# Kernel optimization log

Measured on AMD Instinct MI355X. Metric: run time of the kernel, lower is better.

Reference implementation:

```python
import jax, jax.numpy as jnp
import numpy as np

USER = 100000
ITEM = 50000
N = USER + ITEM
LATDIM = 64
IMG_DIM = 1024
E_ADJ = 3_000_000
E_IMG = 1_000_000
GNN_LAYERS = 2
RIS_LAMBDA = 1.0
EPS = 1e-12


def spmm(rows, cols, vals, x):
    # sparse [N,N] @ dense [N,D] via gather + segment-sum
    return jax.ops.segment_sum(vals[:, None] * x[cols], rows, num_segments=N)


def setup_inputs() -> dict:
    key = jax.random.key(0)
    ks = jax.random.split(key, 10)
    return {
        "adj_rows": jax.random.randint(ks[0], (E_ADJ,), 0, N, dtype=jnp.int32),
        "adj_cols": jax.random.randint(ks[1], (E_ADJ,), 0, N, dtype=jnp.int32),
        "adj_vals": jax.random.uniform(ks[2], (E_ADJ,), dtype=jnp.float32),
        "img_rows": jax.random.randint(ks[3], (E_IMG,), 0, N, dtype=jnp.int32),
        "img_cols": jax.random.randint(ks[4], (E_IMG,), 0, N, dtype=jnp.int32),
        "img_vals": jax.random.uniform(ks[5], (E_IMG,), dtype=jnp.float32),
        "image_embedding": jax.random.normal(ks[6], (ITEM, IMG_DIM), dtype=jnp.float32),
        "uEmbeds": jax.random.normal(ks[7], (USER, LATDIM), dtype=jnp.float32) * 0.01,
        "iEmbeds": jax.random.normal(ks[8], (ITEM, LATDIM), dtype=jnp.float32) * 0.01,
        "W_trans": jax.random.normal(ks[9], (IMG_DIM, LATDIM), dtype=jnp.float32) * (1.0 / np.sqrt(IMG_DIM)),
        "b_trans": jnp.zeros((LATDIM,), dtype=jnp.float32),
    }


def reference(adj_rows, adj_cols, adj_vals, img_rows, img_cols, img_vals,
              image_embedding, uEmbeds, iEmbeds, W_trans, b_trans):
    # trans == 1: Linear projection of image features
    image_feats = image_embedding @ W_trans + b_trans  # [ITEM, LATDIM]

    # image_adj @ concat(u, i)
    embeds_img_adj = spmm(img_rows, img_cols, img_vals, jnp.concatenate([uEmbeds, iEmbeds], axis=0))

    # F.normalize(image_feats) along dim=1 (L2, eps=1e-12)
    nrm = jnp.linalg.norm(image_feats, axis=1, keepdims=True)
    feats_n = image_feats / jnp.maximum(nrm, EPS)

    embeds_image = spmm(adj_rows, adj_cols, adj_vals, jnp.concatenate([uEmbeds, feats_n], axis=0))
    embeds_image_ = spmm(adj_rows, adj_cols, adj_vals,
                         jnp.concatenate([embeds_image[:USER], iEmbeds], axis=0))
    embeds_image = embeds_image + embeds_image_ + RIS_LAMBDA * embeds_img_adj

    # stacked GCN layers with sum over all layer outputs (including input)
    acc = embeds_image
    cur = embeds_image
    for _ in range(GNN_LAYERS):
        cur = spmm(adj_rows, adj_cols, adj_vals, cur)
        acc = acc + cur

    return acc[:USER], acc[USER:]
```

## Files before the change

kernel.cpp:

```cpp
#include <hip/hip_runtime.h>
#include <hip/hip_fp16.h>

#define USER_N 100000
#define ITEM_N 50000
#define NN (USER_N + ITEM_N)
#define D 64
#define IMGD 1024
#define LDP 68
#define KSPLIT 4
#define KQ (IMGD / KSPLIT)

#define BUCKET_BITS 10
#define BROWS (1 << BUCKET_BITS)
#define NBUCK ((NN + BROWS - 1) >> BUCKET_BITS)
#define CHUNK 4096

typedef _Float16 v4h __attribute__((ext_vector_type(4)));
typedef _Float16 v8h __attribute__((ext_vector_type(8)));
typedef float v4f __attribute__((ext_vector_type(4)));

typedef __attribute__((address_space(1))) unsigned int GU32;
typedef __attribute__((address_space(3))) unsigned int LU32;

__global__ __launch_bounds__(256) void prep_fused(
    const float* __restrict__ uE, const float* __restrict__ iE,
    __half* __restrict__ x0, __half* __restrict__ xBI,
    const float* __restrict__ W, _Float16* __restrict__ Wt16, int cvt_blocks)
{
    if (blockIdx.x < cvt_blocks) {
        const int i = blockIdx.x * 256 + threadIdx.x;
        const int n4u = USER_N * D / 4;
        const int n4 = NN * D / 4;
        if (i >= n4) return;
        const float4 v = (i < n4u) ? reinterpret_cast<const float4*>(uE)[i]
                                   : reinterpret_cast<const float4*>(iE)[i - n4u];
        union { uint2 u2; __half2 h[2]; } o;
        o.h[0] = __floats2half2_rn(v.x, v.y);
        o.h[1] = __floats2half2_rn(v.z, v.w);
        *reinterpret_cast<uint2*>(x0 + (size_t)i * 4) = o.u2;
        if (i >= n4u)
            *reinterpret_cast<uint2*>(xBI + (size_t)(i - n4u) * 4) = o.u2;
    } else {
        const int id = (blockIdx.x - cvt_blocks) * 256 + threadIdx.x;
        if (id >= D * IMGD) return;
        const int c = id >> 10;
        const int k = id & 1023;
        Wt16[id] = (_Float16)W[(size_t)k * D + c];
    }
}

__global__ __launch_bounds__(256) void gemm_g(
    const float* __restrict__ A, const _Float16* __restrict__ Wt16,
    float* __restrict__ P0, float* __restrict__ P123,
    const int* __restrict__ rp, const int2* __restrict__ ev,
    const __half* __restrict__ src, float* __restrict__ out32,
    int gemm_blocks, int g_blocks)
{
    __shared__ float As[32 * KQ];
    const int q = blockIdx.x / 7, r7 = blockIdx.x % 7;
    if (r7 < 4) {
        const int gb = q * 4 + r7;
        if (gb >= gemm_blocks) return;
        const int t = threadIdx.x;
        const int w = t >> 6;
        const int lane = t & 63;
        const int l16 = lane & 15;
        const int g = lane >> 4;
        const int tile = gb >> 2;
        const int ks = gb & 3;
        const int row0 = tile * 32;
        const int kbase = ks * KQ;

#pragma unroll
        for (int i = 0; i < 8; i++) {
            const int r = w * 8 + i;
            const int grow = row0 + r;
            const int garow = grow < ITEM_N ? grow : ITEM_N - 1;
            const int xm = (r & 7) << 4;
            const char* srcp = reinterpret_cast<const char*>(
                A + (size_t)garow * IMGD + kbase) + ((lane * 16) ^ xm);
            __builtin_amdgcn_global_load_lds(
                (GU32*)srcp, (LU32*)&As[r * KQ], 16, 0, 0);
        }
        asm volatile("s_waitcnt vmcnt(0)" ::: "memory");
        __syncthreads();

        const int wr = (w >> 1) * 16;
        const int wc = (w & 1) * 32;
        const int rr = wr + l16;
        const char* rbase = reinterpret_cast<const char*>(&As[rr * KQ]);
        const int xm = (rr & 7) << 4;

        v4f acc[2] = {};
        const _Float16* wb = Wt16 + (size_t)l16 * IMGD + kbase + g * 4;

        for (int c = 0; c < KQ; c += 64) {
            const int cb = c * 4;
            const float4 f0 = *reinterpret_cast<const float4*>(rbase + ((cb + g * 16) ^ xm));
            const float4 f1 = *reinterpret_cast<const float4*>(rbase + ((cb + 64 + g * 16) ^ xm));
            const float4 f2 = *reinterpret_cast<const float4*>(rbase + ((cb + 128 + g * 16) ^ xm));
            const float4 f3 = *reinterpret_cast<const float4*>(rbase + ((cb + 192 + g * 16) ^ xm));
            union { v8h v; v4h h[2]; } af0, af1;
            {
                v4h h;
                h[0] = (_Float16)f0.x; h[1] = (_Float16)f0.y;
                h[2] = (_Float16)f0.z; h[3] = (_Float16)f0.w;
                af0.h[0] = h;
                h[0] = (_Float16)f1.x; h[1] = (_Float16)f1.y;
                h[2] = (_Float16)f1.z; h[3] = (_Float16)f1.w;
                af0.h[1] = h;
                h[0] = (_Float16)f2.x; h[1] = (_Float16)f2.y;
                h[2] = (_Float16)f2.z; h[3] = (_Float16)f2.w;
                af1.h[0] = h;
                h[0] = (_Float16)f3.x; h[1] = (_Float16)f3.y;
                h[2] = (_Float16)f3.z; h[3] = (_Float16)f3.w;
                af1.h[1] = h;
            }
#pragma unroll
            for (int n = 0; n < 2; n++) {
                const _Float16* wp = wb + (size_t)(wc + n * 16) * IMGD + c;
                union { v8h v; v4h h[2]; } bf;
                bf.h[0] = *reinterpret_cast<const v4h*>(wp);
                bf.h[1] = *reinterpret_cast<const v4h*>(wp + 16);
                acc[n] = __builtin_amdgcn_mfma_f32_16x16x32_f16(af0.v, bf.v, acc[n], 0, 0, 0);
                bf.h[0] = *reinterpret_cast<const v4h*>(wp + 32);
                bf.h[1] = *reinterpret_cast<const v4h*>(wp + 48);
                acc[n] = __builtin_amdgcn_mfma_f32_16x16x32_f16(af1.v, bf.v, acc[n], 0, 0, 0);
            }
        }
        float* Cp = (ks == 0) ? P0 : P123 + (size_t)(ks - 1) * ITEM_N * D;
#pragma unroll
        for (int n = 0; n < 2; n++) {
            const int col = wc + n * 16 + l16;
#pragma unroll
            for (int r = 0; r < 4; r++) {
                const int grow = row0 + wr + g * 4 + r;
                if (grow < ITEM_N)
                    Cp[(size_t)grow * D + col] = acc[n][r];
            }
        }
    } else {
        const int sb = q * 3 + (r7 - 4);
        if (sb >= g_blocks) return;
        const int wid = (sb * 256 + threadIdx.x) >> 6;
        const int lane = threadIdx.x & 63;
        const int sub = lane >> 3;
        const int l8 = lane & 7;
        const int rowbase = wid * 8;
        if (rowbase >= NN) return;
        const int row = rowbase + sub;

        int v = 0;
        if (lane <= 8 && rowbase + lane <= NN) v = rp[rowbase + lane];
        const int s = __shfl(v, sub, 64);
        const int e = __shfl(v, sub + 1, 64);

        const __half* srcl = src + l8 * 8;
        float acc[8] = {};

        union cvt4 { uint4 u; __half2 h[4]; };
        int i = s;
        for (; i + 3 < e; i += 4) {
            const int2 E0 = ev[i], E1 = ev[i + 1], E2 = ev[i + 2], E3 = ev[i + 3];
            cvt4 g0, g1, g2, g3;
            g0.u = *reinterpret_cast<const uint4*>(srcl + (size_t)E0.x * D);
            g1.u = *reinterpret_cast<const uint4*>(srcl + (size_t)E1.x * D);
            g2.u = *reinterpret_cast<const uint4*>(srcl + (size_t)E2.x * D);
            g3.u = *reinterpret_cast<const uint4*>(srcl + (size_t)E3.x * D);
#pragma unroll
            for (int k = 0; k < 4; k++) {
                const cvt4& g = k == 0 ? g0 : k == 1 ? g1 : k == 2 ? g2 : g3;
                const float w = __int_as_float(k == 0 ? E0.y : k == 1 ? E1.y
                                               : k == 2 ? E2.y : E3.y);
#pragma unroll
                for (int j = 0; j < 4; j++) {
                    const float2 f = __half22float2(g.h[j]);
                    acc[2 * j]     += w * f.x;
                    acc[2 * j + 1] += w * f.y;
                }
            }
        }
        for (; i < e; i++) {
            const int2 E0 = ev[i];
            cvt4 g;
            g.u = *reinterpret_cast<const uint4*>(srcl + (size_t)E0.x * D);
            const float w = __int_as_float(E0.y);
#pragma unroll
            for (int j = 0; j < 4; j++) {
                const float2 f = __half22float2(g.h[j]);
                acc[2 * j]     += w * f.x;
                acc[2 * j + 1] += w * f.y;
            }
        }

        if (row >= NN) return;
        const size_t idx = (size_t)row * D + l8 * 8;
#pragma unroll
        for (int h = 0; h < 2; h++) {
            float4 o;
            o.x = acc[4 * h]; o.y = acc[4 * h + 1];
            o.z = acc[4 * h + 2]; o.w = acc[4 * h + 3];
            *reinterpret_cast<float4*>(&out32[idx + h * 4]) = o;
        }
    }
}

__global__ __launch_bounds__(256) void gemm_feats32(
    const float* __restrict__ A, const float* __restrict__ W,
    const float* __restrict__ b, float* __restrict__ C)
{
    __shared__ float As[32][LDP];
    __shared__ float Ws[64][LDP];
    const int row0 = blockIdx.x * 32;
    const int t = threadIdx.x;
    const int tx = t & 15, ty = t >> 4;
    float acc[2][4] = {};

    const int lr = t >> 4;
    const int lk = (t & 15) * 4;

    for (int k0 = 0; k0 < IMGD; k0 += 64) {
#pragma unroll
        for (int i = 0; i < 2; i++) {
            const int r = lr + i * 16;
            const int grow = row0 + r;
            float4 v = make_float4(0.f, 0.f, 0.f, 0.f);
            if (grow < ITEM_N)
                v = *reinterpret_cast<const float4*>(&A[(size_t)grow * IMGD + k0 + lk]);
            *reinterpret_cast<float4*>(&As[r][lk]) = v;
        }
#pragma unroll
        for (int i = 0; i < 4; i++) {
            const int kr = lr + i * 16;
            float4 v = *reinterpret_cast<const float4*>(&W[(size_t)(k0 + kr) * D + lk]);
            *reinterpret_cast<float4*>(&Ws[kr][lk]) = v;
        }
        __syncthreads();
#pragma unroll
        for (int kb = 0; kb < 16; kb++) {
            float a_[2][4], w_[4][4];
#pragma unroll
            for (int i = 0; i < 2; i++) {
                const float4 v = *reinterpret_cast<const float4*>(&As[ty * 2 + i][kb * 4]);
                a_[i][0] = v.x; a_[i][1] = v.y; a_[i][2] = v.z; a_[i][3] = v.w;
            }
#pragma unroll
            for (int j = 0; j < 4; j++) {
                const float4 v = *reinterpret_cast<const float4*>(&Ws[kb * 4 + j][tx * 4]);
                w_[j][0] = v.x; w_[j][1] = v.y; w_[j][2] = v.z; w_[j][3] = v.w;
            }
#pragma unroll
            for (int j = 0; j < 4; j++)
#pragma unroll
                for (int i = 0; i < 2; i++)
#pragma unroll
                    for (int c = 0; c < 4; c++)
                        acc[i][c] += a_[i][j] * w_[j][c];
        }
        __syncthreads();
    }
    const float4 bias = *reinterpret_cast<const float4*>(&b[tx * 4]);
#pragma unroll
    for (int i = 0; i < 2; i++) {
        const int grow = row0 + ty * 2 + i;
        if (grow < ITEM_N) {
            float4 v;
            v.x = acc[i][0] + bias.x;
            v.y = acc[i][1] + bias.y;
            v.z = acc[i][2] + bias.z;
            v.w = acc[i][3] + bias.w;
            *reinterpret_cast<float4*>(&C[(size_t)grow * D + tx * 4]) = v;
        }
    }
}

__global__ __launch_bounds__(256) void rownorm_h4(
    const float* __restrict__ P0, const float* __restrict__ P123,
    const float* __restrict__ b, __half* __restrict__ Y, int nrows)
{
    const int gid = blockIdx.x * blockDim.x + threadIdx.x;
    const int row = gid >> 6;
    const int lane = threadIdx.x & 63;
    if (row >= nrows) return;
    const size_t idx = (size_t)row * D + lane;
    const size_t N1 = (size_t)ITEM_N * D;
    float v = P0[idx] + P123[idx] + P123[idx + N1] + P123[idx + 2 * N1] + b[lane];
    float s = v * v;
#pragma unroll
    for (int o = 32; o > 0; o >>= 1) s += __shfl_xor(s, o, 64);
    const float scale = 1.0f / fmaxf(sqrtf(s), 1e-12f);
    Y[idx] = __float2half(v * scale);
}

__global__ __launch_bounds__(256) void rownorm(float* __restrict__ X, int nrows)
{
    const int gid = blockIdx.x * blockDim.x + threadIdx.x;
    const int row = gid >> 6;
    const int lane = threadIdx.x & 63;
    if (row >= nrows) return;
    float v = X[(size_t)row * D + lane];
    float s = v * v;
#pragma unroll
    for (int o = 32; o > 0; o >>= 1) s += __shfl_xor(s, o, 64);
    const float scale = 1.0f / fmaxf(sqrtf(s), 1e-12f);
    X[(size_t)row * D + lane] = v * scale;
}

__global__ __launch_bounds__(256) void bucket_count2(
    const int* __restrict__ rows_a, int nnz_a, int nb_a, int* __restrict__ histT_a,
    const int* __restrict__ rows_b, int nnz_b, int nb_b, int* __restrict__ histT_b)
{
    const bool isA = (int)blockIdx.x < nb_a;
    const int bid = isA ? blockIdx.x : blockIdx.x - nb_a;
    const int* rows = isA ? rows_a : rows_b;
    const int nnz = isA ? nnz_a : nnz_b;
    const int nb = isA ? nb_a : nb_b;
    int* histT = isA ? histT_a : histT_b;

    __shared__ int cnt[NBUCK];
    for (int i = threadIdx.x; i < NBUCK; i += 256) cnt[i] = 0;
    __syncthreads();
    const int e0 = bid * CHUNK;
    const int e1 = min(e0 + CHUNK, nnz);
    for (int e = e0 + threadIdx.x; e < e1; e += 256)
        atomicAdd(&cnt[rows[e] >> BUCKET_BITS], 1);
    __syncthreads();
    for (int b = threadIdx.x; b < NBUCK; b += 256)
        histT[b * nb + bid] = cnt[b];
}

__global__ __launch_bounds__(1024) void scanA2(
    int* __restrict__ histTA, int* __restrict__ bsumsA, int nA, int nsbA,
    int* __restrict__ histTB, int* __restrict__ bsumsB, int nB)
{
    const bool isA = (int)blockIdx.x < nsbA;
    int* cnt = isA ? histTA : histTB;
    int* bsums = isA ? bsumsA : bsumsB;
    const int n = isA ? nA : nB;
    const int bid = isA ? blockIdx.x : blockIdx.x - nsbA;

    const int t = threadIdx.x;
    const int gid = bid * 1024 + t;
    const int lane = t & 63, wid = t >> 6;
    int v = (gid < n) ? cnt[gid] : 0;
    int x = v;
#pragma unroll
    for (int o = 1; o < 64; o <<= 1) {
        int y = __shfl_up(x, o, 64);
        if (lane >= o) x += y;
    }
    __shared__ int ws[16];
    __shared__ int wo[16];
    if (lane == 63) ws[wid] = x;
    __syncthreads();
    if (t < 16) {
        int s = ws[t];
        int xx = s;
#pragma unroll
        for (int o = 1; o < 16; o <<= 1) {
            int y = __shfl_up(xx, o, 16);
            if (t >= o) xx += y;
        }
        wo[t] = xx - s;
        if (t == 15) bsums[bid] = xx;
    }
    __syncthreads();
    if (gid < n) cnt[gid] = x - v + wo[wid];
}

__global__ __launch_bounds__(1024) void scanB2(
    int* __restrict__ bsA, int nbA, int* __restrict__ bsB, int nbB)
{
    int* bs = blockIdx.x == 0 ? bsA : bsB;
    const int nb = blockIdx.x == 0 ? nbA : nbB;
    const int t = threadIdx.x;
    const int lane = t & 63, wid = t >> 6;
    int v = (t < nb) ? bs[t] : 0;
    int x = v;
#pragma unroll
    for (int o = 1; o < 64; o <<= 1) {
        int y = __shfl_up(x, o, 64);
        if (lane >= o) x += y;
    }
    __shared__ int ws[16];
    __shared__ int wo[16];
    if (lane == 63) ws[wid] = x;
    __syncthreads();
    if (t < 16) {
        int s = ws[t];
        int xx = s;
#pragma unroll
        for (int o = 1; o < 16; o <<= 1) {
            int y = __shfl_up(xx, o, 16);
            if (t >= o) xx += y;
        }
        wo[t] = xx - s;
    }
    __syncthreads();
    if (t < nb) bs[t] = x - v + wo[wid];
}

__global__ __launch_bounds__(256) void scan_apply2(
    int* __restrict__ histTA, const int* __restrict__ bsA, int nA,
    int* __restrict__ histTB, const int* __restrict__ bsB, int nB)
{
    const int gid = blockIdx.x * blockDim.x + threadIdx.x;
    if (gid < nA) histTA[gid] += bsA[gid >> 10];
    else if (gid - nA < nB) histTB[gid - nA] += bsB[(gid - nA) >> 10];
}

__global__ __launch_bounds__(256) void bucket_place2(
    const int* __restrict__ rows_a, const int* __restrict__ cols_a,
    const float* __restrict__ vals_a, int nnz_a, int nb_a,
    const int* __restrict__ offsT_a, uint2* __restrict__ rec_a,
    const int* __restrict__ rows_b, const int* __restrict__ cols_b,
    const float* __restrict__ vals_b, int nnz_b, int nb_b,
    const int* __restrict__ offsT_b, uint2* __restrict__ rec_b)
{
    const bool isA = (int)blockIdx.x < nb_a;
    const int bid = isA ? blockIdx.x : blockIdx.x - nb_a;
    const int* rows = isA ? rows_a : rows_b;
    const int* cols = isA ? cols_a : cols_b;
    const float* vals = isA ? vals_a : vals_b;
    const int nnz = isA ? nnz_a : nnz_b;
    const int nb = isA ? nb_a : nb_b;
    const int* offsT = isA ? offsT_a : offsT_b;
    uint2* rec = isA ? rec_a : rec_b;

    __shared__ int cur[NBUCK];
    for (int b = threadIdx.x; b < NBUCK; b += 256)
        cur[b] = offsT[b * nb + bid];
    __syncthreads();
    const int e0 = bid * CHUNK;
    const int e1 = min(e0 + CHUNK, nnz);
    for (int e = e0 + threadIdx.x; e < e1; e += 256) {
        const int r = rows[e];
        const int b = r >> BUCKET_BITS;
        const int pos = atomicAdd(&cur[b], 1);
        rec[pos] = make_uint2(((unsigned)cols[e] << BUCKET_BITS) |
                                  (unsigned)(r & (BROWS - 1)),
                              __float_as_uint(vals[e]));
    }
}

__global__ __launch_bounds__(1024) void bucket_finalize2(
    const uint2* __restrict__ rec_a, int nnz_a, int nb_a,
    const int* __restrict__ offsT_a, int* __restrict__ rp_a, int2* __restrict__ ev_a,
    const uint2* __restrict__ rec_b, int nnz_b, int nb_b,
    const int* __restrict__ offsT_b, int* __restrict__ rp_b, int2* __restrict__ ev_b)
{
    const bool isA = (int)blockIdx.x < NBUCK;
    const int b = isA ? blockIdx.x : blockIdx.x - NBUCK;
    const uint2* rec = isA ? rec_a : rec_b;
    const int nnz = isA ? nnz_a : nnz_b;
    const int nb = isA ? nb_a : nb_b;
    const int* offsT = isA ? offsT_a : offsT_b;
    int* rp = isA ? rp_a : rp_b;
    int2* ev = isA ? ev_a : ev_b;

    const int t = threadIdx.x;
    const int rlo = b << BUCKET_BITS;
    const int segs = offsT[b * nb];
    const int sege = (b + 1 < NBUCK) ? offsT[(b + 1) * nb] : nnz;

    __shared__ int cnt[BROWS];
    __shared__ int cur[BROWS];
    cnt[t] = 0;
    __syncthreads();
    for (int i = segs + t; i < sege; i += 1024)
        atomicAdd(&cnt[rec[i].x & (BROWS - 1)], 1);
    __syncthreads();

    const int lane = t & 63, wid = t >> 6;
    const int v = cnt[t];
    int x = v;
#pragma unroll
    for (int o = 1; o < 64; o <<= 1) {
        int y = __shfl_up(x, o, 64);
        if (lane >= o) x += y;
    }
    __shared__ int wsum[16];
    __shared__ int woff[16];
    if (lane == 63) wsum[wid] = x;
    __syncthreads();
    if (t < 16) {
        int s = wsum[t];
        int xx = s;
#pragma unroll
        for (int o = 1; o < 16; o <<= 1) {
            int y = __shfl_up(xx, o, 16);
            if (t >= o) xx += y;
        }
        woff[t] = xx - s;
    }
    __syncthreads();
    const int start = segs + (x - v + woff[wid]);

    if (rlo + t < NN) rp[rlo + t] = start;
    if (b == NBUCK - 1 && t == 0) rp[NN] = nnz;
    cur[t] = start;
    __syncthreads();

    for (int i = segs + t; i < sege; i += 1024) {
        const uint2 R = rec[i];
        const int rl = (int)(R.x & (BROWS - 1));
        const int c = (int)(R.x >> BUCKET_BITS);
        const int pos = atomicAdd(&cur[rl], 1);
        ev[pos] = make_int2(c, (int)R.y);
    }
}

__global__ __launch_bounds__(256) void spmm_h8(
    const int* __restrict__ rp, const int2* __restrict__ ev,
    const __half* __restrict__ src,
    float* __restrict__ out32, __half* __restrict__ out16, int limit16,
    const float* __restrict__ add1, const float* __restrict__ add2)
{
    const int wid = (blockIdx.x * 256 + threadIdx.x) >> 6;
    const int lane = threadIdx.x & 63;
    const int sub = lane >> 3;
    const int l8 = lane & 7;
    const int rowbase = wid * 8;
    if (rowbase >= NN) return;
    const int row = rowbase + sub;

    int v = 0;
    if (lane <= 8 && rowbase + lane <= NN) v = rp[rowbase + lane];
    const int s = __shfl(v, sub, 64);
    const int e = __shfl(v, sub + 1, 64);

    const __half* srcl = src + l8 * 8;
    float acc[8] = {};

    union cvt4 { uint4 u; __half2 h[4]; };
    int i = s;
    for (; i + 3 < e; i += 4) {
        const int2 E0 = ev[i], E1 = ev[i + 1], E2 = ev[i + 2], E3 = ev[i + 3];
        cvt4 g0, g1, g2, g3;
        g0.u = *reinterpret_cast<const uint4*>(srcl + (size_t)E0.x * D);
        g1.u = *reinterpret_cast<const uint4*>(srcl + (size_t)E1.x * D);
        g2.u = *reinterpret_cast<const uint4*>(srcl + (size_t)E2.x * D);
        g3.u = *reinterpret_cast<const uint4*>(srcl + (size_t)E3.x * D);
#pragma unroll
        for (int k = 0; k < 4; k++) {
            const cvt4& g = k == 0 ? g0 : k == 1 ? g1 : k == 2 ? g2 : g3;
            const float w = __int_as_float(k == 0 ? E0.y : k == 1 ? E1.y
                                           : k == 2 ? E2.y : E3.y);
#pragma unroll
            for (int j = 0; j < 4; j++) {
                const float2 f = __half22float2(g.h[j]);
                acc[2 * j]     += w * f.x;
                acc[2 * j + 1] += w * f.y;
            }
        }
    }
    for (; i < e; i++) {
        const int2 E0 = ev[i];
        cvt4 g;
        g.u = *reinterpret_cast<const uint4*>(srcl + (size_t)E0.x * D);
        const float w = __int_as_float(E0.y);
#pragma unroll
        for (int j = 0; j < 4; j++) {
            const float2 f = __half22float2(g.h[j]);
            acc[2 * j]     += w * f.x;
            acc[2 * j + 1] += w * f.y;
        }
    }

    if (row >= NN) return;
    const size_t idx = (size_t)row * D + l8 * 8;
#pragma unroll
    for (int h = 0; h < 2; h++) {
        if (add1) {
            const float4 a = *reinterpret_cast<const float4*>(&add1[idx + h * 4]);
            acc[4 * h] += a.x; acc[4 * h + 1] += a.y;
            acc[4 * h + 2] += a.z; acc[4 * h + 3] += a.w;
        }
        if (add2) {
            const float4 a = *reinterpret_cast<const float4*>(&add2[idx + h * 4]);
            acc[4 * h] += a.x; acc[4 * h + 1] += a.y;
            acc[4 * h + 2] += a.z; acc[4 * h + 3] += a.w;
        }
        float4 o;
        o.x = acc[4 * h]; o.y = acc[4 * h + 1];
        o.z = acc[4 * h + 2]; o.w = acc[4 * h + 3];
        *reinterpret_cast<float4*>(&out32[idx + h * 4]) = o;
    }
    if (row < limit16) {
        cvt4 o16;
#pragma unroll
        for (int j = 0; j < 4; j++)
            o16.h[j] = __floats2half2_rn(acc[2 * j], acc[2 * j + 1]);
        *reinterpret_cast<uint4*>(&out16[idx]) = o16.u;
    }
}

__global__ __launch_bounds__(256) void spmm_csr(
    const int* __restrict__ rp, const int2* __restrict__ ev,
    const float* __restrict__ srcU, const float* __restrict__ srcI,
    float* __restrict__ out,
    const float* __restrict__ add1, const float* __restrict__ add2)
{
    const int gid = blockIdx.x * blockDim.x + threadIdx.x;
    const int row = gid >> 6;
    const int lane = threadIdx.x & 63;
    if (row >= NN) return;
    const int s = rp[row], e = rp[row + 1];
    float acc = 0.f;
    int i = s;
    for (; i + 3 < e; i += 4) {
        const int2 e0 = ev[i], e1 = ev[i + 1], e2 = ev[i + 2], e3 = ev[i + 3];
        const float* p0 = (e0.x < USER_N) ? (srcU + (size_t)e0.x * D)
                                          : (srcI + (size_t)(e0.x - USER_N) * D);
        const float* p1 = (e1.x < USER_N) ? (srcU + (size_t)e1.x * D)
                                          : (srcI + (size_t)(e1.x - USER_N) * D);
        const float* p2 = (e2.x < USER_N) ? (srcU + (size_t)e2.x * D)
                                          : (srcI + (size_t)(e2.x - USER_N) * D);
        const float* p3 = (e3.x < USER_N) ? (srcU + (size_t)e3.x * D)
                                          : (srcI + (size_t)(e3.x - USER_N) * D);
        acc += __int_as_float(e0.y) * p0[lane];
        acc += __int_as_float(e1.y) * p1[lane];
        acc += __int_as_float(e2.y) * p2[lane];
        acc += __int_as_float(e3.y) * p3[lane];
    }
    for (; i < e; i++) {
        const int2 e0 = ev[i];
        const float* p0 = (e0.x < USER_N) ? (srcU + (size_t)e0.x * D)
                                          : (srcI + (size_t)(e0.x - USER_N) * D);
        acc += __int_as_float(e0.y) * p0[lane];
    }
    const size_t idx = (size_t)row * D + lane;
    if (add1) acc += add1[idx];
    if (add2) acc += add2[idx];
    out[idx] = acc;
}

extern "C" void kernel_launch(void* const* d_in, const int* in_sizes, int n_in,
                              void* d_out, int out_size, void* d_ws, size_t ws_size,
                              hipStream_t stream)
{
    const int*   adj_rows = (const int*)d_in[0];
    const int*   adj_cols = (const int*)d_in[1];
    const float* adj_vals = (const float*)d_in[2];
    const int*   img_rows = (const int*)d_in[3];
    const int*   img_cols = (const int*)d_in[4];
    const float* img_vals = (const float*)d_in[5];
    const float* img_emb  = (const float*)d_in[6];
    const float* uEmb     = (const float*)d_in[7];
    const float* iEmb     = (const float*)d_in[8];
    const float* Wt       = (const float*)d_in[9];
    const float* bt       = (const float*)d_in[10];
    float* out = (float*)d_out;

    const int e_adj = in_sizes[0];
    const int e_img = in_sizes[3];
    const int e_max = e_adj > e_img ? e_adj : e_img;
    const int NB_adj = (e_adj + CHUNK - 1) / CHUNK;
    const int NB_img = (e_img + CHUNK - 1) / CHUNK;

    const size_t ndbytes = (size_t)NN * D * sizeof(float);
    const size_t nhbytes = (size_t)NN * D * sizeof(__half);

    size_t off = 0;
    auto carve = [&](size_t bytes) { size_t p = off; off += (bytes + 255) & ~(size_t)255; return p; };
    char* base = (char*)d_ws;
    const size_t o_featsN = carve((size_t)ITEM_N * D * sizeof(float));
    const size_t o_bufA   = carve(ndbytes);
    const size_t o_bufB   = carve(ndbytes);
    const size_t o_rpAdj  = carve((NN + 1) * sizeof(int));
    const size_t o_rpImg  = carve((NN + 1) * sizeof(int));
    const size_t o_bsumsA = carve(1024 * sizeof(int));
    const size_t o_bsumsB = carve(1024 * sizeof(int));
    const size_t o_histTA = carve((size_t)NBUCK * NB_adj * sizeof(int));
    const size_t o_histTB = carve((size_t)NBUCK * NB_img * sizeof(int));
    const size_t o_recA   = carve((size_t)e_max * sizeof(uint2) > nhbytes
                                      ? (size_t)e_max * sizeof(uint2) : nhbytes);
    const size_t o_evAdj  = carve((size_t)e_adj * sizeof(int2));
    const size_t need_base = off;
    const size_t o_evImg  = carve((size_t)e_img * sizeof(int2) > nhbytes
                                      ? (size_t)e_img * sizeof(int2) : nhbytes);
    const size_t o_x0     = carve((size_t)e_img * sizeof(uint2) > nhbytes
                                      ? (size_t)e_img * sizeof(uint2) : nhbytes);
    const size_t o_wt16   = carve((size_t)D * IMGD * sizeof(_Float16));
    const size_t need_h = off;

    if (ws_size < need_base) return;
    const bool use_h = (ws_size >= need_h);

    float* featsN = (float*)(base + o_featsN);
    float* bufA   = (float*)(base + o_bufA);
    float* bufB   = (float*)(base + o_bufB);
    int* rpAdj    = (int*)(base + o_rpAdj);
    int* rpImg    = (int*)(base + o_rpImg);
    int* bsumsA   = (int*)(base + o_bsumsA);
    int* bsumsB   = (int*)(base + o_bsumsB);
    int* histTA   = (int*)(base + o_histTA);
    int* histTB   = (int*)(base + o_histTB);
    uint2* recA   = (uint2*)(base + o_recA);
    uint2* recB   = (uint2*)(base + o_x0);
    int2* evAdj   = (int2*)(base + o_evAdj);
    int2* evImg   = (int2*)(base + o_evImg);
    __half* xC    = (__half*)(base + o_recA);
    __half* xB    = (__half*)(base + o_evImg);
    __half* x0    = (__half*)(base + o_x0);
    _Float16* wt16 = (_Float16*)(base + o_wt16);

    const int SPMM8_GRID = (NN + 31) / 32;
    const int SPMM_GRID = (NN * 64 + 255) / 256;
    const int RN_GRID = (ITEM_N * 64 + 255) / 256;
    const int GEMM_BLOCKS = ((ITEM_N + 31) / 32) * KSPLIT;
    const int MEGA_GRID = 1563 * 7;

    const int nA = NBUCK * NB_adj, nsbA = (nA + 1023) / 1024;
    const int nB = NBUCK * NB_img, nsbB = (nB + 1023) / 1024;
    bucket_count2<<<NB_adj + NB_img, 256, 0, stream>>>(
        adj_rows, e_adj, NB_adj, histTA, img_rows, e_img, NB_img, histTB);
    scanA2<<<nsbA + nsbB, 1024, 0, stream>>>(
        histTA, bsumsA, nA, nsbA, histTB, bsumsB, nB);
    scanB2<<<2, 1024, 0, stream>>>(bsumsA, nsbA, bsumsB, nsbB);
    scan_apply2<<<(nA + nB + 255) / 256, 256, 0, stream>>>(
        histTA, bsumsA, nA, histTB, bsumsB, nB);
    bucket_place2<<<NB_adj + NB_img, 256, 0, stream>>>(
        adj_rows, adj_cols, adj_vals, e_adj, NB_adj, histTA, recA,
        img_rows, img_cols, img_vals, e_img, NB_img, histTB, recB);
    bucket_finalize2<<<2 * NBUCK, 1024, 0, stream>>>(
        recA, e_adj, NB_adj, histTA, rpAdj, evAdj,
        recB, e_img, NB_img, histTB, rpImg, evImg);

    if (use_h) {
        __half* x0I = x0 + (size_t)USER_N * D;
        __half* xBI = xB + (size_t)USER_N * D;

        const int CVT_BLOCKS = (NN * D / 4 + 255) / 256;
        prep_fused<<<CVT_BLOCKS + (D * IMGD + 255) / 256, 256, 0, stream>>>(
            uEmb, iEmb, x0, xBI, Wt, wt16, CVT_BLOCKS);

        gemm_g<<<MEGA_GRID, 256, 0, stream>>>(
            img_emb, wt16, featsN, bufB, rpImg, evImg, x0, bufA,
            GEMM_BLOCKS, SPMM8_GRID);

        rownorm_h4<<<RN_GRID, 256, 0, stream>>>(featsN, bufB, bt, x0I, ITEM_N);

        spmm_h8<<<SPMM8_GRID, 256, 0, stream>>>(
            rpAdj, evAdj, x0, bufB, xB, USER_N, nullptr, nullptr);

        spmm_h8<<<SPMM8_GRID, 256, 0, stream>>>(
            rpAdj, evAdj, xB, bufA, xC, NN, bufB, bufA);

        spmm_h8<<<SPMM8_GRID, 256, 0, stream>>>(
            rpAdj, evAdj, xC, bufB, x0, NN, nullptr, nullptr);

        spmm_h8<<<SPMM8_GRID, 256, 0, stream>>>(
            rpAdj, evAdj, x0, out, nullptr, 0, bufA, bufB);
    } else {
        gemm_feats32<<<(ITEM_N + 31) / 32, 256, 0, stream>>>(img_emb, Wt, bt, featsN);
        rownorm<<<RN_GRID, 256, 0, stream>>>(featsN, ITEM_N);

        spmm_csr<<<SPMM_GRID, 256, 0, stream>>>(
            rpImg, evImg, uEmb, iEmb, bufA, nullptr, nullptr);
        spmm_csr<<<SPMM_GRID, 256, 0, stream>>>(
            rpAdj, evAdj, uEmb, featsN, bufB, nullptr, nullptr);
        spmm_csr<<<SPMM_GRID, 256, 0, stream>>>(
            rpAdj, evAdj, bufB, iEmb, bufA, bufB, bufA);
        spmm_csr<<<SPMM_GRID, 256, 0, stream>>>(
            rpAdj, evAdj, bufA, bufA + (size_t)USER_N * D, bufB, nullptr, nullptr);
        spmm_csr<<<SPMM_GRID, 256, 0, stream>>>(
            rpAdj, evAdj, bufB, bufB + (size_t)USER_N * D, out, bufA, bufB);
    }
}
```

Measured before the change: 560.7 us.

## Split first adjacency SpMM by column range to overlap user part with GEMM

Within each CSR row, adjacency edges are now sorted so user-column edges come first, with a split pointer per row. The user-column partial SpMM does not depend on the projected image features, so it moves into the merged GEMM/SpMM kernel as extra blocks and writes a half-precision partial. A new fix-up kernel then adds the item-column contributions after the row normalisation. This overlaps about two thirds of the first propagation with the GEMM. In exchange it adds an extra fp16 rounding of the partial, more shared atomics during finalize, and a larger grid.

```diff
diff --git a/kernel.cpp b/kernel.cpp
--- a/kernel.cpp
+++ b/kernel.cpp
@@ -52,14 +52,18 @@
 __global__ __launch_bounds__(256) void gemm_g(
     const float* __restrict__ A, const _Float16* __restrict__ Wt16,
     float* __restrict__ P0, float* __restrict__ P123,
-    const int* __restrict__ rp, const int2* __restrict__ ev,
+    const int* __restrict__ rpI, const int2* __restrict__ evI,
+    const int* __restrict__ rpA, const int* __restrict__ spA,
+    const int2* __restrict__ evA,
     const __half* __restrict__ src, float* __restrict__ out32,
+    __half* __restrict__ e1p,
     int gemm_blocks, int g_blocks)
 {
     __shared__ float As[32 * KQ];
-    const int q = blockIdx.x / 7, r7 = blockIdx.x % 7;
-    if (r7 < 4) {
-        const int gb = q * 4 + r7;
+    const int q = blockIdx.x / 10, r10 = blockIdx.x % 10;
+    union cvt4 { uint4 u; __half2 h[4]; };
+    if (r10 < 4) {
+        const int gb = q * 4 + r10;
         if (gb >= gemm_blocks) return;
         const int t = threadIdx.x;
         const int w = t >> 6;
@@ -139,8 +143,8 @@
                     Cp[(size_t)grow * D + col] = acc[n][r];
             }
         }
-    } else {
-        const int sb = q * 3 + (r7 - 4);
+    } else if (r10 < 7) {
+        const int sb = q * 3 + (r10 - 4);
         if (sb >= g_blocks) return;
         const int wid = (sb * 256 + threadIdx.x) >> 6;
         const int lane = threadIdx.x & 63;
@@ -151,17 +155,16 @@
         const int row = rowbase + sub;
 
         int v = 0;
-        if (lane <= 8 && rowbase + lane <= NN) v = rp[rowbase + lane];
+        if (lane <= 8 && rowbase + lane <= NN) v = rpI[rowbase + lane];
         const int s = __shfl(v, sub, 64);
         const int e = __shfl(v, sub + 1, 64);
 
         const __half* srcl = src + l8 * 8;
         float acc[8] = {};
 
-        union cvt4 { uint4 u; __half2 h[4]; };
         int i = s;
         for (; i + 3 < e; i += 4) {
-            const int2 E0 = ev[i], E1 = ev[i + 1], E2 = ev[i + 2], E3 = ev[i + 3];
+            const int2 E0 = evI[i], E1 = evI[i + 1], E2 = evI[i + 2], E3 = evI[i + 3];
             cvt4 g0, g1, g2, g3;
             g0.u = *reinterpret_cast<const uint4*>(srcl + (size_t)E0.x * D);
             g1.u = *reinterpret_cast<const uint4*>(srcl + (size_t)E1.x * D);
@@ -181,7 +184,7 @@
             }
         }
         for (; i < e; i++) {
-            const int2 E0 = ev[i];
+            const int2 E0 = evI[i];
             cvt4 g;
             g.u = *reinterpret_cast<const uint4*>(srcl + (size_t)E0.x * D);
             const float w = __int_as_float(E0.y);
@@ -202,6 +205,154 @@
             o.z = acc[4 * h + 2]; o.w = acc[4 * h + 3];
             *reinterpret_cast<float4*>(&out32[idx + h * 4]) = o;
         }
+    } else {
+        const int sb = q * 3 + (r10 - 7);
+        if (sb >= g_blocks) return;
+        const int wid = (sb * 256 + threadIdx.x) >> 6;
+        const int lane = threadIdx.x & 63;
+        const int sub = lane >> 3;
+        const int l8 = lane & 7;
+        const int rowbase = wid * 8;
+        if (rowbase >= NN) return;
+        const int row = rowbase + sub;
+
+        int v = 0, u = 0;
+        if (lane <= 8 && rowbase + lane <= NN) v = rpA[rowbase + lane];
+        if (lane < 8 && rowbase + lane < NN) u = spA[rowbase + lane];
+        const int s = __shfl(v, sub, 64);
+        const int e = __shfl(u, sub, 64);
+
+        const __half* srcl = src + l8 * 8;
+        float acc[8] = {};
+
+        int i = s;
+        for (; i + 3 < e; i += 4) {
+            const int2 E0 = evA[i], E1 = evA[i + 1], E2 = evA[i + 2], E3 = evA[i + 3];
+            cvt4 g0, g1, g2, g3;
+            g0.u = *reinterpret_cast<const uint4*>(srcl + (size_t)E0.x * D);
+            g1.u = *reinterpret_cast<const uint4*>(srcl + (size_t)E1.x * D);
+            g2.u = *reinterpret_cast<const uint4*>(srcl + (size_t)E2.x * D);
+            g3.u = *reinterpret_cast<const uint4*>(srcl + (size_t)E3.x * D);
+#pragma unroll
+            for (int k = 0; k < 4; k++) {
+                const cvt4& g = k == 0 ? g0 : k == 1 ? g1 : k == 2 ? g2 : g3;
+                const float w = __int_as_float(k == 0 ? E0.y : k == 1 ? E1.y
+                                               : k == 2 ? E2.y : E3.y);
+#pragma unroll
+                for (int j = 0; j < 4; j++) {
+                    const float2 f = __half22float2(g.h[j]);
+                    acc[2 * j]     += w * f.x;
+                    acc[2 * j + 1] += w * f.y;
+                }
+            }
+        }
+        for (; i < e; i++) {
+            const int2 E0 = evA[i];
+            cvt4 g;
+            g.u = *reinterpret_cast<const uint4*>(srcl + (size_t)E0.x * D);
+            const float w = __int_as_float(E0.y);
+#pragma unroll
+            for (int j = 0; j < 4; j++) {
+                const float2 f = __half22float2(g.h[j]);
+                acc[2 * j]     += w * f.x;
+                acc[2 * j + 1] += w * f.y;
+            }
+        }
+
+        if (row >= NN) return;
+        const size_t idx = (size_t)row * D + l8 * 8;
+        cvt4 o16;
+#pragma unroll
+        for (int j = 0; j < 4; j++)
+            o16.h[j] = __floats2half2_rn(acc[2 * j], acc[2 * j + 1]);
+        *reinterpret_cast<uint4*>(&e1p[idx]) = o16.u;
+    }
+}
+
+__global__ __launch_bounds__(256) void spmm_fix(
+    const int* __restrict__ rp, const int* __restrict__ sp,
+    const int2* __restrict__ ev, const __half* __restrict__ src,
+    const __half* __restrict__ partial,
+    float* __restrict__ out32, __half* __restrict__ out16, int limit16)
+{
+    const int wid = (blockIdx.x * 256 + threadIdx.x) >> 6;
+    const int lane = threadIdx.x & 63;
+    const int sub = lane >> 3;
+    const int l8 = lane & 7;
+    const int rowbase = wid * 8;
+    if (rowbase >= NN) return;
+    const int row = rowbase + sub;
+
+    int v = 0, u = 0;
+    if (lane <= 8 && rowbase + lane <= NN) v = rp[rowbase + lane];
+    if (lane < 8 && rowbase + lane < NN) u = sp[rowbase + lane];
+    const int s = __shfl(u, sub, 64);
+    const int e = __shfl(v, sub + 1, 64);
+
+    const __half* srcl = src + l8 * 8;
+    float acc[8];
+    union cvt4 { uint4 u; __half2 h[4]; };
+    {
+        const size_t idx0 = (size_t)((row < NN) ? row : 0) * D + l8 * 8;
+        cvt4 p;
+        p.u = *reinterpret_cast<const uint4*>(&partial[idx0]);
+#pragma unroll
+        for (int j = 0; j < 4; j++) {
+            const float2 f = __half22float2(p.h[j]);
+            acc[2 * j] = f.x;
+            acc[2 * j + 1] = f.y;
+        }
+    }
+
+    int i = s;
+    for (; i + 3 < e; i += 4) {
+        const int2 E0 = ev[i], E1 = ev[i + 1], E2 = ev[i + 2], E3 = ev[i + 3];
+        cvt4 g0, g1, g2, g3;
+        g0.u = *reinterpret_cast<const uint4*>(srcl + (size_t)E0.x * D);
+        g1.u = *reinterpret_cast<const uint4*>(srcl + (size_t)E1.x * D);
+        g2.u = *reinterpret_cast<const uint4*>(srcl + (size_t)E2.x * D);
+        g3.u = *reinterpret_cast<const uint4*>(srcl + (size_t)E3.x * D);
+#pragma unroll
+        for (int k = 0; k < 4; k++) {
+            const cvt4& g = k == 0 ? g0 : k == 1 ? g1 : k == 2 ? g2 : g3;
+            const float w = __int_as_float(k == 0 ? E0.y : k == 1 ? E1.y
+                                           : k == 2 ? E2.y : E3.y);
+#pragma unroll
+            for (int j = 0; j < 4; j++) {
+                const float2 f = __half22float2(g.h[j]);
+                acc[2 * j]     += w * f.x;
+                acc[2 * j + 1] += w * f.y;
+            }
+        }
+    }
+    for (; i < e; i++) {
+        const int2 E0 = ev[i];
+        cvt4 g;
+        g.u = *reinterpret_cast<const uint4*>(srcl + (size_t)E0.x * D);
+        const float w = __int_as_float(E0.y);
+#pragma unroll
+        for (int j = 0; j < 4; j++) {
+            const float2 f = __half22float2(g.h[j]);
+            acc[2 * j]     += w * f.x;
+            acc[2 * j + 1] += w * f.y;
+        }
+    }
+
+    if (row >= NN) return;
+    const size_t idx = (size_t)row * D + l8 * 8;
+#pragma unroll
+    for (int h = 0; h < 2; h++) {
+        float4 o;
+        o.x = acc[4 * h]; o.y = acc[4 * h + 1];
+        o.z = acc[4 * h + 2]; o.w = acc[4 * h + 3];
+        *reinterpret_cast<float4*>(&out32[idx + h * 4]) = o;
+    }
+    if (row < limit16) {
+        cvt4 o16;
+#pragma unroll
+        for (int j = 0; j < 4; j++)
+            o16.h[j] = __floats2half2_rn(acc[2 * j], acc[2 * j + 1]);
+        *reinterpret_cast<uint4*>(&out16[idx]) = o16.u;
     }
 }
 
@@ -446,6 +597,7 @@
 __global__ __launch_bounds__(1024) void bucket_finalize2(
     const uint2* __restrict__ rec_a, int nnz_a, int nb_a,
     const int* __restrict__ offsT_a, int* __restrict__ rp_a, int2* __restrict__ ev_a,
+    int* __restrict__ sp_a,
     const uint2* __restrict__ rec_b, int nnz_b, int nb_b,
     const int* __restrict__ offsT_b, int* __restrict__ rp_b, int2* __restrict__ ev_b)
 {
@@ -464,11 +616,18 @@
     const int sege = (b + 1 < NBUCK) ? offsT[(b + 1) * nb] : nnz;
 
     __shared__ int cnt[BROWS];
-    __shared__ int cur[BROWS];
+    __shared__ int cntU[BROWS];
+    __shared__ int curU[BROWS];
+    __shared__ int curI[BROWS];
     cnt[t] = 0;
-    __syncthreads();
-    for (int i = segs + t; i < sege; i += 1024)
-        atomicAdd(&cnt[rec[i].x & (BROWS - 1)], 1);
+    cntU[t] = 0;
+    __syncthreads();
+    for (int i = segs + t; i < sege; i += 1024) {
+        const unsigned x = rec[i].x;
+        const int rl = (int)(x & (BROWS - 1));
+        atomicAdd(&cnt[rl], 1);
+        if ((int)(x >> BUCKET_BITS) < USER_N) atomicAdd(&cntU[rl], 1);
+    }
     __syncthreads();
 
     const int lane = t & 63, wid = t >> 6;
@@ -496,16 +655,20 @@
     __syncthreads();
     const int start = segs + (x - v + woff[wid]);
 
-    if (rlo + t < NN) rp[rlo + t] = start;
+    if (rlo + t < NN) {
+        rp[rlo + t] = start;
+        if (isA) sp_a[rlo + t] = start + cntU[t];
+    }
     if (b == NBUCK - 1 && t == 0) rp[NN] = nnz;
-    cur[t] = start;
+    curU[t] = start;
+    curI[t] = start + cntU[t];
     __syncthreads();
 
     for (int i = segs + t; i < sege; i += 1024) {
         const uint2 R = rec[i];
         const int rl = (int)(R.x & (BROWS - 1));
         const int c = (int)(R.x >> BUCKET_BITS);
-        const int pos = atomicAdd(&cur[rl], 1);
+        const int pos = atomicAdd((c < USER_N) ? &curU[rl] : &curI[rl], 1);
         ev[pos] = make_int2(c, (int)R.y);
     }
 }
@@ -669,6 +832,7 @@
     const size_t o_bufB   = carve(ndbytes);
     const size_t o_rpAdj  = carve((NN + 1) * sizeof(int));
     const size_t o_rpImg  = carve((NN + 1) * sizeof(int));
+    const size_t o_spAdj  = carve((NN + 1) * sizeof(int));
     const size_t o_bsumsA = carve(1024 * sizeof(int));
     const size_t o_bsumsB = carve(1024 * sizeof(int));
     const size_t o_histTA = carve((size_t)NBUCK * NB_adj * sizeof(int));
@@ -692,6 +856,7 @@
     float* bufB   = (float*)(base + o_bufB);
     int* rpAdj    = (int*)(base + o_rpAdj);
     int* rpImg    = (int*)(base + o_rpImg);
+    int* spAdj    = (int*)(base + o_spAdj);
     int* bsumsA   = (int*)(base + o_bsumsA);
     int* bsumsB   = (int*)(base + o_bsumsB);
     int* histTA   = (int*)(base + o_histTA);
@@ -709,10 +874,16 @@
     const int SPMM_GRID = (NN * 64 + 255) / 256;
     const int RN_GRID = (ITEM_N * 64 + 255) / 256;
     const int GEMM_BLOCKS = ((ITEM_N + 31) / 32) * KSPLIT;
-    const int MEGA_GRID = 1563 * 7;
+    const int MEGA_GRID = 1563 * 10;
 
     const int nA = NBUCK * NB_adj, nsbA = (nA + 1023) / 1024;
     const int nB = NBUCK * NB_img, nsbB = (nB + 1023) / 1024;
+    const int CVT_BLOCKS = (NN * D / 4 + 255) / 256;
+    const int WT_BLOCKS = (D * IMGD + 255) / 256;
+
+    __half* x0I = x0 + (size_t)USER_N * D;
+    __half* xBI = xB + (size_t)USER_N * D;
+
     bucket_count2<<<NB_adj + NB_img, 256, 0, stream>>>(
         adj_rows, e_adj, NB_adj, histTA, img_rows, e_img, NB_img, histTB);
     scanA2<<<nsbA + nsbB, 1024, 0, stream>>>(
@@ -724,25 +895,22 @@
         adj_rows, adj_cols, adj_vals, e_adj, NB_adj, histTA, recA,
         img_rows, img_cols, img_vals, e_img, NB_img, histTB, recB);
     bucket_finalize2<<<2 * NBUCK, 1024, 0, stream>>>(
-        recA, e_adj, NB_adj, histTA, rpAdj, evAdj,
+        recA, e_adj, NB_adj, histTA, rpAdj, evAdj, spAdj,
         recB, e_img, NB_img, histTB, rpImg, evImg);
 
     if (use_h) {
-        __half* x0I = x0 + (size_t)USER_N * D;
-        __half* xBI = xB + (size_t)USER_N * D;
-
-        const int CVT_BLOCKS = (NN * D / 4 + 255) / 256;
-        prep_fused<<<CVT_BLOCKS + (D * IMGD + 255) / 256, 256, 0, stream>>>(
+        prep_fused<<<CVT_BLOCKS + WT_BLOCKS, 256, 0, stream>>>(
             uEmb, iEmb, x0, xBI, Wt, wt16, CVT_BLOCKS);
 
         gemm_g<<<MEGA_GRID, 256, 0, stream>>>(
-            img_emb, wt16, featsN, bufB, rpImg, evImg, x0, bufA,
+            img_emb, wt16, featsN, bufB, rpImg, evImg,
+            rpAdj, spAdj, evAdj, x0, bufA, xC,
             GEMM_BLOCKS, SPMM8_GRID);
 
         rownorm_h4<<<RN_GRID, 256, 0, stream>>>(featsN, bufB, bt, x0I, ITEM_N);
 
-        spmm_h8<<<SPMM8_GRID, 256, 0, stream>>>(
-            rpAdj, evAdj, x0, bufB, xB, USER_N, nullptr, nullptr);
+        spmm_fix<<<SPMM8_GRID, 256, 0, stream>>>(
+            rpAdj, spAdj, evAdj, x0, xC, bufB, xB, USER_N);
 
         spmm_h8<<<SPMM8_GRID, 256, 0, stream>>>(
             rpAdj, evAdj, xB, bufA, xC, NN, bufB, bufA);
```

After: 568.0 us. About the same (+1.3%).
